# Kernel tuning notes

Hardware: AMD Instinct MI355X
Metric: run time of the kernel (lower is better)

The kernel has to match this reference:

```python
import jax, jax.numpy as jnp
import numpy as np

B, N, D = 32, 2048, 16
PCD = 2        # point_cloud_dimensions
K_NN = 16      # k nearest neighbours
FILTERS = 64


def setup_inputs() -> dict:
    key = jax.random.key(0)
    k1, k2, k3 = jax.random.split(key, 3)
    x = jax.random.normal(k1, (B, N, D), dtype=jnp.float32)
    # 1x1 Conv2D == dense over the last (channel) dim: W [D, FILTERS], b [FILTERS]
    W = jax.random.normal(k2, (D, FILTERS), dtype=jnp.float32) * (1.0 / np.sqrt(D))
    b = jnp.zeros((FILTERS,), dtype=jnp.float32)
    return {"x": x, "W": W, "b": b}


def reference(x, W, b):
    # points = first PCD channels; features = full input (dynamic_coordinates=True)
    points = x[:, :, :PCD]                                   # [B,N,PCD]
    # squared pairwise distances: ||p_i||^2 + ||p_j||^2 - 2 p_i.p_j  -> [B,N,N]
    sq = jnp.sum(points * points, axis=-1)                   # [B,N]
    dist = sq[:, :, None] + sq[:, None, :] - 2.0 * jnp.einsum(
        'bnd,bmd->bnm', points, points)
    # k nearest neighbours (smallest distance) per point -> [B,N,k]
    _, idx = jax.lax.top_k(-dist, K_NN)
    # gather neighbour features: [B,N,k,D]
    neigh = jax.vmap(lambda f, i: f[i])(x, idx)
    centre = x[:, :, None, :]                                # [B,N,1,D]
    # NOTE: source concatenates along the neighbour axis -> [B,N,k+1,D]
    edges = jnp.concatenate([centre, neigh - centre], axis=2)
    # 1x1 conv (linear activation) over channel dim: [B,N,k+1,FILTERS]
    conv = jnp.einsum('bnkd,df->bnkf', edges, W) + b
    # Max pooling over neighbour axis: [B,N,FILTERS]
    pooled = jnp.max(conv, axis=2)
    # shortcut_input_features=True: concat original features
    return jnp.concatenate([pooled, x], axis=-1)             # [B,N,FILTERS+D]
```

## Files before the change

### kernel.cpp

```cpp
#include <hip/hip_runtime.h>


#define B_  32
#define N_  2048
#define D_  16
#define F_  64
#define K_  16
#define OUTD (F_ + D_)
#define NQ  64
#define NS  4
#define SPLIT (N_ / NS)

__global__ __launch_bounds__(256) void proj_kernel(const float* __restrict__ x,
                                                   const float* __restrict__ W,
                                                   float* __restrict__ Y) {
    __shared__ float Ws[D_ * F_];
    __shared__ float xs[16][D_];
    const int t = threadIdx.x;
    for (int i = t; i < D_ * F_; i += 256) Ws[i] = W[i];
    const int p0 = blockIdx.x * 16;
    ((float*)xs)[t] = x[(size_t)p0 * D_ + t];
    __syncthreads();
    const int w = t >> 6, f = t & 63;
#pragma unroll
    for (int i = 0; i < 4; i++) {
        const int pw = w * 4 + i;
        float acc = 0.f;
#pragma unroll
        for (int d = 0; d < D_; d++) acc = fmaf(xs[pw][d], Ws[d * F_ + f], acc);
        Y[(size_t)(p0 + pw) * F_ + f] = acc;
    }
}

__global__ __launch_bounds__(256, 4) void knn_kernel(const float* __restrict__ x,
                                                     int* __restrict__ idx) {
    __shared__ float2 pts[N_];
    __shared__ float  sqs[N_];
    __shared__ float  arr_raw[NS - 1][NQ * 17];
    __shared__ float  Tq[NQ];
    __shared__ int    cnt[NQ];
    __shared__ int    tiecnt[NS][NQ];
    unsigned short (*tiebuf)[NQ][K_] =
        (unsigned short (*)[NQ][K_])&arr_raw[0][0];

    const int b = blockIdx.x >> 5;
    const int qbase = (blockIdx.x & 31) * NQ;
    const int t = threadIdx.x;
    const int s = t >> 6;
    const int qi = t & 63;
    const int q = qbase + qi;

    const float* xb = x + (size_t)b * N_ * D_;
    for (int m = t; m < N_; m += 256) {
        float2 p = make_float2(xb[m * D_ + 0], xb[m * D_ + 1]);
        pts[m] = p;
        sqs[m] = __fadd_rn(__fmul_rn(p.x, p.x), __fmul_rn(p.y, p.y));
    }
    if (t < NQ) cnt[t] = 0;
    __syncthreads();

    const float2 qp = pts[q];
    const float sqn = sqs[q];

    float key[K_];
#pragma unroll
    for (int j = 0; j < K_; j++) key[j] = INFINITY;

    const int m0 = s * SPLIT, m1 = m0 + SPLIT;
#pragma unroll 2
    for (int m = m0; m < m1; m += 2) {
        float2 pa = pts[m];     float sa = sqs[m];
        float2 pb = pts[m + 1]; float sb = sqs[m + 1];
        float dota = __fmaf_rn(qp.y, pa.y, __fmul_rn(qp.x, pa.x));
        float da   = __fsub_rn(__fadd_rn(sqn, sa), __fmul_rn(2.f, dota));
        float dotb = __fmaf_rn(qp.y, pb.y, __fmul_rn(qp.x, pb.x));
        float db   = __fsub_rn(__fadd_rn(sqn, sb), __fmul_rn(2.f, dotb));
        float y0 = fminf(da, db), y1 = fmaxf(da, db);
#pragma unroll
        for (int j = K_ - 1; j >= 2; j--)
            key[j] = fminf(fminf(key[j], fmaxf(key[j - 1], y0)),
                           fmaxf(key[j - 2], y1));
        key[1] = fminf(fminf(key[1], fmaxf(key[0], y0)), y1);
        key[0] = fminf(key[0], y0);
    }

    if (s > 0) {
#pragma unroll
        for (int j = 0; j < K_; j++) arr_raw[s - 1][qi * 17 + j] = key[j];
    }
    __syncthreads();

    if (s == 0) {
        for (int ss = 0; ss < NS - 1; ss++) {
#pragma unroll
            for (int j = 0; j < K_; j += 2) {
                float y0 = arr_raw[ss][qi * 17 + j];
                float y1 = arr_raw[ss][qi * 17 + j + 1];
#pragma unroll
                for (int jj = K_ - 1; jj >= 2; jj--)
                    key[jj] = fminf(fminf(key[jj], fmaxf(key[jj - 1], y0)),
                                    fmaxf(key[jj - 2], y1));
                key[1] = fminf(fminf(key[1], fmaxf(key[0], y0)), y1);
                key[0] = fminf(key[0], y0);
            }
        }
        Tq[qi] = key[K_ - 1];
    }
    __syncthreads();

    const float T = Tq[qi];
    int* op = idx + ((size_t)b * N_ + q) * K_;
    int tc = 0;
    for (int m = m0; m < m1; m++) {
        float2 p = pts[m];
        float dot = __fmaf_rn(qp.y, p.y, __fmul_rn(qp.x, p.x));
        float d   = __fsub_rn(__fadd_rn(sqn, sqs[m]), __fmul_rn(2.f, dot));
        if (d < T) {
            int slot = atomicAdd(&cnt[qi], 1);
            op[slot] = m;
        } else if (d == T) {
            if (tc < K_) tiebuf[s][qi][tc] = (unsigned short)m;
            tc++;
        }
    }
    tiecnt[s][qi] = (tc < K_) ? tc : K_;
    __syncthreads();

    if (s == 0) {
        int c1 = cnt[qi];
        int w = c1;
        int need = K_ - c1;
        for (int ss = 0; ss < NS && need > 0; ss++) {
            int nn = tiecnt[ss][qi];
            for (int j = 0; j < nn && need > 0; j++) {
                op[w++] = (int)tiebuf[ss][qi][j];
                need--;
            }
        }
    }
}

__global__ __launch_bounds__(256) void pool_kernel(const float* __restrict__ x,
                                                   const float* __restrict__ bias,
                                                   const float* __restrict__ Y,
                                                   const int* __restrict__ idx,
                                                   float* __restrict__ out) {
    const int t = threadIdx.x;
    const int w = t >> 6, f = t & 63;
    const float bf = bias[f];
#pragma unroll
    for (int i = 0; i < 4; i++) {
        const int p = blockIdx.x * 16 + w * 4 + i;
        const int b = p >> 11;
        const size_t pb = (size_t)p;

        const float yn = Y[pb * F_ + f];
        const int* ip = idx + pb * K_;
        float M = -INFINITY;
#pragma unroll
        for (int k = 0; k < K_; k++) {
            int m = ip[k];
            float ym = Y[((size_t)b * N_ + m) * F_ + f];
            M = fmaxf(M, ym);
        }
        float pooled = fmaxf(yn, M - yn) + bf;
        out[pb * OUTD + f] = pooled;
        if (f < D_) out[pb * OUTD + F_ + f] = x[pb * D_ + f];
    }
}

extern "C" void kernel_launch(void* const* d_in, const int* in_sizes, int n_in,
                              void* d_out, int out_size, void* d_ws, size_t ws_size,
                              hipStream_t stream) {
    const float* x    = (const float*)d_in[0];
    const float* W    = (const float*)d_in[1];
    const float* bias = (const float*)d_in[2];
    float* out = (float*)d_out;

    float* Y  = (float*)d_ws;
    int*  idx = (int*)((char*)d_ws + (size_t)B_ * N_ * F_ * 4);

    proj_kernel<<<B_ * N_ / 16, 256, 0, stream>>>(x, W, Y);
    knn_kernel <<<B_ * (N_ / NQ), 256, 0, stream>>>(x, idx);
    pool_kernel<<<B_ * N_ / 16, 256, 0, stream>>>(x, bias, Y, idx, out);
}
```

Measured before the change: 290.0 us.

## Fuse max-pool gather into kNN kernel using shared-memory neighbour indices

The pooling step now runs at the end of the kNN kernel. Neighbour indices stay in shared memory (in the spare space of the merge buffer) and are no longer written to and read back from a global idx array, which also removes one kernel launch. Each block then gathers the projected features for its 64 queries, with one thread per filter. The unroll factors of both distance loops are raised as well. The cost is that the gather and pool work now runs at the kNN kernel's occupancy, with 16 queries handled serially per wave.

```diff
diff --git a/kernel.cpp b/kernel.cpp
--- a/kernel.cpp
+++ b/kernel.cpp
@@ -33,7 +33,9 @@
 }
 
 __global__ __launch_bounds__(256, 4) void knn_kernel(const float* __restrict__ x,
-                                                     int* __restrict__ idx) {
+                                                     const float* __restrict__ bias,
+                                                     const float* __restrict__ Y,
+                                                     float* __restrict__ out) {
     __shared__ float2 pts[N_];
     __shared__ float  sqs[N_];
     __shared__ float  arr_raw[NS - 1][NQ * 17];
@@ -42,6 +44,7 @@
     __shared__ int    tiecnt[NS][NQ];
     unsigned short (*tiebuf)[NQ][K_] =
         (unsigned short (*)[NQ][K_])&arr_raw[0][0];
+    int (*idxL)[K_] = (int (*)[K_])((char*)&arr_raw[0][0] + 8192);
 
     const int b = blockIdx.x >> 5;
     const int qbase = (blockIdx.x & 31) * NQ;
@@ -67,7 +70,7 @@
     for (int j = 0; j < K_; j++) key[j] = INFINITY;
 
     const int m0 = s * SPLIT, m1 = m0 + SPLIT;
-#pragma unroll 2
+#pragma unroll 4
     for (int m = m0; m < m1; m += 2) {
         float2 pa = pts[m];     float sa = sqs[m];
         float2 pb = pts[m + 1]; float sb = sqs[m + 1];
@@ -109,15 +112,15 @@
     __syncthreads();
 
     const float T = Tq[qi];
-    int* op = idx + ((size_t)b * N_ + q) * K_;
     int tc = 0;
+#pragma unroll 2
     for (int m = m0; m < m1; m++) {
         float2 p = pts[m];
         float dot = __fmaf_rn(qp.y, p.y, __fmul_rn(qp.x, p.x));
         float d   = __fsub_rn(__fadd_rn(sqn, sqs[m]), __fmul_rn(2.f, dot));
         if (d < T) {
             int slot = atomicAdd(&cnt[qi], 1);
-            op[slot] = m;
+            idxL[qi][slot] = m;
         } else if (d == T) {
             if (tc < K_) tiebuf[s][qi][tc] = (unsigned short)m;
             tc++;
@@ -133,39 +136,29 @@
         for (int ss = 0; ss < NS && need > 0; ss++) {
             int nn = tiecnt[ss][qi];
             for (int j = 0; j < nn && need > 0; j++) {
-                op[w++] = (int)tiebuf[ss][qi][j];
+                idxL[qi][w++] = (int)tiebuf[ss][qi][j];
                 need--;
             }
         }
     }
-}
+    __syncthreads();
 
-__global__ __launch_bounds__(256) void pool_kernel(const float* __restrict__ x,
-                                                   const float* __restrict__ bias,
-                                                   const float* __restrict__ Y,
-                                                   const int* __restrict__ idx,
-                                                   float* __restrict__ out) {
-    const int t = threadIdx.x;
-    const int w = t >> 6, f = t & 63;
+    const int f = qi;
     const float bf = bias[f];
-#pragma unroll
-    for (int i = 0; i < 4; i++) {
-        const int p = blockIdx.x * 16 + w * 4 + i;
-        const int b = p >> 11;
-        const size_t pb = (size_t)p;
-
-        const float yn = Y[pb * F_ + f];
-        const int* ip = idx + pb * K_;
+    const float* Yb = Y + (size_t)b * N_ * F_;
+    for (int i = 0; i < 16; i++) {
+        const int qq = s * 16 + i;
+        const int gq = qbase + qq;
+        const float yn = Yb[(size_t)gq * F_ + f];
         float M = -INFINITY;
 #pragma unroll
         for (int k = 0; k < K_; k++) {
-            int m = ip[k];
-            float ym = Y[((size_t)b * N_ + m) * F_ + f];
-            M = fmaxf(M, ym);
+            int m = idxL[qq][k];
+            M = fmaxf(M, Yb[(size_t)m * F_ + f]);
         }
-        float pooled = fmaxf(yn, M - yn) + bf;
-        out[pb * OUTD + f] = pooled;
-        if (f < D_) out[pb * OUTD + F_ + f] = x[pb * D_ + f];
+        const size_t pb = (size_t)b * N_ + gq;
+        out[pb * OUTD + f] = fmaxf(yn, M - yn) + bf;
+        if (f < D_) out[pb * OUTD + F_ + f] = xb[(size_t)gq * D_ + f];
     }
 }
 
@@ -177,10 +170,8 @@
     const float* bias = (const float*)d_in[2];
     float* out = (float*)d_out;
 
-    float* Y  = (float*)d_ws;
-    int*  idx = (int*)((char*)d_ws + (size_t)B_ * N_ * F_ * 4);
+    float* Y = (float*)d_ws;
 
     proj_kernel<<<B_ * N_ / 16, 256, 0, stream>>>(x, W, Y);
-    knn_kernel <<<B_ * (N_ / NQ), 256, 0, stream>>>(x, idx);
-    pool_kernel<<<B_ * N_ / 16, 256, 0, stream>>>(x, bias, Y, idx, out);
+    knn_kernel <<<B_ * (N_ / NQ), 256, 0, stream>>>(x, bias, Y, out);
 }
```

New measurement: 259.4 us. -10.6%, faster.
